# Kernel optimization log

Hardware: AMD Instinct MI355X
Metric: run time of the kernel (lower is better)

## Reference

```python
import jax, jax.numpy as jnp
import numpy as np

DIM = 64      # GCM input_dim
H = DIM // 2  # per-branch width
B = 4         # batch samples
NP = 50000    # points per sample
G = 128       # voxel grid extent
N = B * NP


def _build_coords_and_neighbors():
    rng = np.random.default_rng(0)
    coords = []
    for b in range(B):
        flat = rng.choice(G ** 3, size=NP, replace=False)
        cz = flat % G
        cy = (flat // G) % G
        cx = flat // (G * G)
        coords.append(np.stack([cx, cy, cz], axis=1))
    coords = np.concatenate(coords, axis=0).astype(np.int64)  # [N,3]
    batch_id = np.repeat(np.arange(B), NP).astype(np.int64)
    key = ((batch_id * G + coords[:, 0]) * G + coords[:, 1]) * G + coords[:, 2]
    order = np.argsort(key)
    skey = key[order]
    offs = [(dx, dy, dz) for dx in (-1, 0, 1) for dy in (-1, 0, 1) for dz in (-1, 0, 1)]
    nbr = np.full((27, N), -1, dtype=np.int32)
    for k, (dx, dy, dz) in enumerate(offs):
        nx = coords[:, 0] + dx; ny = coords[:, 1] + dy; nz = coords[:, 2] + dz
        valid = (nx >= 0) & (nx < G) & (ny >= 0) & (ny < G) & (nz >= 0) & (nz < G)
        nkey = ((batch_id * G + nx) * G + ny) * G + nz
        pos = np.searchsorted(skey, nkey)
        pos_c = np.clip(pos, 0, N - 1)
        found = valid & (skey[pos_c] == nkey)
        nbr[k] = np.where(found, order[pos_c], -1).astype(np.int32)
    return nbr, batch_id.astype(np.int32)


def setup_inputs() -> dict:
    nbr, batch_id = _build_coords_and_neighbors()
    key = jax.random.key(0)
    ks = jax.random.split(key, 12)
    sc3 = 1.0 / np.sqrt(27 * H)
    sc1d = 1.0 / np.sqrt(DIM)
    sc1h = 1.0 / np.sqrt(H)
    f32 = jnp.float32
    return {
        "x_feats": jax.random.normal(ks[0], (N, DIM), f32),
        "Wg1": jax.random.normal(ks[1], (DIM, DIM), f32) * sc1d,
        "bg1": jnp.zeros((DIM,), f32),
        "Wg2": jax.random.normal(ks[2], (DIM, DIM), f32) * sc1d,
        "bg2": jnp.zeros((DIM,), f32),
        "Wr1": jax.random.normal(ks[3], (27, H, H), f32) * sc3,
        "br1": jnp.zeros((H,), f32),
        "Wr2": jax.random.normal(ks[4], (27, H, H), f32) * sc3,
        "br2": jnp.zeros((H,), f32),
        "Wq1": jax.random.normal(ks[5], (27, H, H), f32) * sc3,
        "bq1": jnp.zeros((H,), f32),
        "Wq2": jax.random.normal(ks[6], (27, H, H), f32) * sc3,
        "bq2": jnp.zeros((H,), f32),
        "Wq3": jax.random.normal(ks[7], (H, H), f32) * sc1h,
        "bq3": jnp.zeros((H,), f32),
        "nbr_idx": jnp.asarray(nbr),
        "batch_id": jnp.asarray(batch_id),
        "batch_size": B,
    }


def reference(x_feats, Wg1, bg1, Wg2, bg2, Wr1, br1, Wr2, br2,
              Wq1, bq1, Wq2, bq2, Wq3, bq3, nbr_idx, batch_id, batch_size):
    relu = jax.nn.relu

    def sconv(f, W, b):
        # sparse 3x3x3 conv via precomputed kernel maps: out[i] = sum_k f[nbr[k,i]] @ W[k]
        mask = nbr_idx >= 0                                   # [27,N]
        g = jnp.where(mask[:, :, None], f[jnp.clip(nbr_idx, 0)], 0.0)  # [27,N,Cin]
        return jnp.einsum('knc,kco->no', g, W) + b

    # GCM.conv1 (1x1) then channel split
    y = x_feats @ Wg1 + bg1
    conv_x, glo_x = y[:, :H], y[:, H:]

    # resblock (stride=1, no skip conv) + residual in GCM
    r = relu(sconv(conv_x, Wr1, br1))
    r = relu(sconv(r, Wr2, br2))
    conv_x = (r + conv_x) + conv_x

    # glob_feat
    out1 = relu(sconv(glo_x, Wq1, bq1))
    out2 = relu(sconv(glo_x, Wq2, bq2))
    m1 = jnp.mean(out1, axis=1, keepdims=True)                # [N,1]
    sums = jax.ops.segment_sum(out2, batch_id, num_segments=batch_size)  # [B,H]
    cnts = jax.ops.segment_sum(jnp.ones((out2.shape[0], 1), out2.dtype), batch_id,
                               num_segments=batch_size)
    m2 = sums / cnts                                          # per-sample mean over points
    enc = jnp.sqrt(m1 * m2[batch_id] + 1e-12)                 # per-sample outer product
    f = enc + out1 + out2
    f = relu(f @ Wq3 + bq3)
    glo = relu(glo_x - f)

    # GCM.conv2 (1x1) on channel-concat, residual add
    res = jnp.concatenate([conv_x, glo], axis=1) @ Wg2 + bg2
    return x_feats + res
```

## Files before the change

### kernel.cpp

```cpp
#include <hip/hip_runtime.h>
#include <stdint.h>

typedef unsigned int u32;
typedef unsigned short u16;
typedef unsigned long long u64;
typedef __attribute__((ext_vector_type(8))) short bf16x8;
typedef __attribute__((ext_vector_type(4))) float f32x4;

#define HC 32

__device__ __forceinline__ float u2f(u32 u){ union{u32 i;float f;}v; v.i=u; return v.f; }
__device__ __forceinline__ u16 f2bf(float f){ union{float f;u32 i;}v; v.f=f; u32 i=v.i;
    return (u16)((i + 0x7FFFu + ((i>>16)&1u))>>16); }
__device__ __forceinline__ short bfs(float f){ return (short)f2bf(f); }
__device__ __forceinline__ u32 packbf(float a, float b){ return (u32)f2bf(a) | ((u32)f2bf(b)<<16); }

__global__ __launch_bounds__(256) void k0_prep(
    const float* __restrict__ Wq1, const float* __restrict__ Wq2,
    const float* __restrict__ Wr1, const float* __restrict__ Wr2,
    u16* __restrict__ wsB)
{
    int it = blockIdx.x*256 + threadIdx.x;
    if (it >= 216*64) return;
    int l = it & 63, slot = it >> 6;
    int oh = slot & 1, k = (slot >> 1) % 27, mat = slot / 54;
    const float* W = (mat==0)?Wq1:(mat==1)?Wq2:(mat==2)?Wr1:Wr2;
    const float* src = W + k*1024 + oh*16 + (l & 15);
    int crow = (l >> 4) * 8;
    u32 w4[4];
    #pragma unroll
    for (int jj = 0; jj < 4; ++jj)
        w4[jj] = packbf(src[(crow + 2*jj)*32], src[(crow + 2*jj + 1)*32]);
    *(uint4*)&wsB[slot*512 + l*8] = make_uint4(w4[0], w4[1], w4[2], w4[3]);
}

__global__ __launch_bounds__(256) void k1_mfma(
    const float* __restrict__ x, const float* __restrict__ Wg1, const float* __restrict__ bg1,
    float* __restrict__ cv, float* __restrict__ gl, long long N)
{
    const int lane = threadIdx.x & 63;
    const int m = lane & 15, g = lane >> 4;
    bf16x8 bw[4][2];
    #pragma unroll
    for (int no = 0; no < 4; ++no)
      #pragma unroll
      for (int kf = 0; kf < 2; ++kf)
        #pragma unroll
        for (int j = 0; j < 8; ++j)
            bw[no][kf][j] = bfs(Wg1[(kf*32 + g*8 + j)*64 + no*16 + m]);
    float bias4[4];
    #pragma unroll
    for (int no = 0; no < 4; ++no) bias4[no] = bg1[no*16 + m];

    const long long wave = (long long)blockIdx.x*4 + (threadIdx.x>>6);
    long long t0 = wave * 4;
    #pragma unroll 1
    for (long long t = t0; t < t0+4; ++t) {
        long long p0 = t*16;
        if (p0 >= N) break;
        long long pr_a = p0 + m; if (pr_a > N-1) pr_a = N-1;
        const float4* xr = (const float4*)(x + pr_a*64);
        bf16x8 aw[2];
        #pragma unroll
        for (int kf = 0; kf < 2; ++kf) {
            float4 lo = xr[kf*8 + g*2];
            float4 hi = xr[kf*8 + g*2 + 1];
            aw[kf][0]=bfs(lo.x); aw[kf][1]=bfs(lo.y); aw[kf][2]=bfs(lo.z); aw[kf][3]=bfs(lo.w);
            aw[kf][4]=bfs(hi.x); aw[kf][5]=bfs(hi.y); aw[kf][6]=bfs(hi.z); aw[kf][7]=bfs(hi.w);
        }
        #pragma unroll
        for (int no = 0; no < 4; ++no) {
            f32x4 acc = {0.f,0.f,0.f,0.f};
            acc = __builtin_amdgcn_mfma_f32_16x16x32_bf16(aw[0], bw[no][0], acc, 0,0,0);
            acc = __builtin_amdgcn_mfma_f32_16x16x32_bf16(aw[1], bw[no][1], acc, 0,0,0);
            #pragma unroll
            for (int j = 0; j < 4; ++j) {
                long long pr = p0 + g*4 + j;
                if (pr < N) {
                    float v = acc[j] + bias4[no];
                    if (no < 2) cv[pr*32 + no*16 + m] = v;
                    else        gl[pr*32 + (no-2)*16 + m] = v;
                }
            }
        }
    }
}

__device__ __forceinline__ void load_nbr(
    const int* __restrict__ nbr, long long N, long long p0, int lane, int* nbrv)
{
    #pragma unroll
    for (int ch = 0; ch < 7; ++ch) {
        int i = ch*64 + lane;
        int kk = i >> 4, pp = i & 15;
        nbrv[ch] = (i < 432 && p0 + pp < N) ? nbr[(long long)kk*N + p0 + pp] : -1;
    }
}

__device__ __forceinline__ void enum_tile_reg(
    const int* nbrv,
    u16* plist, int* ilist, u16* slist, u16* sstart,
    int lane, u32& np_out, u32& ns_out)
{
    u32 np = 0, ns = 0;
    #pragma unroll
    for (int ch = 0; ch < 7; ++ch) {
        int i = ch*64 + lane;
        int kk = i >> 4, pp = i & 15;
        int ixv = nbrv[ch];
        u64 b = __ballot(ixv >= 0);
        u32 kact = 0;
        #pragma unroll
        for (int q2 = 0; q2 < 4; ++q2)
            kact |= ((((b >> (16*q2)) & 0xffffull) != 0ull) ? 1u : 0u) << q2;
        if (ixv >= 0) {
            u64 ltm = (1ull << lane) - 1ull;
            u32 pos = np + (u32)__popcll(b & ltm);
            int q2 = lane >> 4;
            u32 s = ns + __popc(kact & ((1u << q2) - 1u));
            if (pos < 224) {
                plist[pos] = (u16)((s << 9) | (u32)pp);
                ilist[pos] = ixv;
                u64 subm = 0xffffull << (16*q2);
                if ((b & subm & ltm) == 0ull) { slist[s] = (u16)kk; sstart[s] = (u16)pos; }
            }
        }
        np += (u32)__popcll(b);
        ns += __popc(kact);
    }
    if (np > 224) np = 224;
    np_out = np; ns_out = ns;
}

template<int KAv>
__device__ __forceinline__ void gather_batch(
    const float* __restrict__ src, u16* A,
    const u16* plist, const int* ilist,
    u32 jS, u32 jE, u32 base, int c32, int hf)
{
    constexpr int STR = KAv*32 + 8;
    constexpr int U4R = KAv*4;
    constexpr int NU4 = 16*U4R;
    const int lane = threadIdx.x & 63;
    uint4 z4 = make_uint4(0u,0u,0u,0u);
    #pragma unroll
    for (int w = 0; w < NU4/64; ++w) {
        int q = w*64 + lane;
        int r = q / U4R, c8 = q - r*U4R;
        *(uint4*)&A[r*STR + c8*8] = z4;
    }
    asm volatile("s_waitcnt lgkmcnt(0)" ::: "memory");
    for (u32 j0 = jS; j0 < jE; j0 += 16) {
        float v[8]; u32 mt[8];
        #pragma unroll
        for (int tt = 0; tt < 8; ++tt) {
            u32 pj = j0 + 2*tt + (u32)hf;
            bool val = pj < jE;
            u32 pm = val ? (u32)plist[pj] : 0u;
            int ix = val ? ilist[pj] : 0;
            mt[tt] = val ? (pm | 0x80000000u) : 0u;
            v[tt] = val ? src[(long long)ix*32 + c32] : 0.f;
        }
        #pragma unroll
        for (int tt = 0; tt < 8; ++tt) {
            if (mt[tt] >> 31) {
                u32 sl = ((mt[tt] >> 9) & 31u) - base;
                u32 p = mt[tt] & 15u;
                A[p*STR + sl*32 + c32] = f2bf(v[tt]);
            }
        }
    }
    asm volatile("s_waitcnt lgkmcnt(0)" ::: "memory");
}

template<int KAv>
__device__ __forceinline__ void gather_batch2(
    const float* __restrict__ src0, const float* __restrict__ src1,
    u16* A0, u16* A1,
    const u16* plist, const int* ilist,
    u32 jS, u32 jE, u32 base, int c32, int hf)
{
    constexpr int STR = KAv*32 + 8;
    constexpr int U4R = KAv*4;
    constexpr int NU4 = 16*U4R;
    const int lane = threadIdx.x & 63;
    uint4 z4 = make_uint4(0u,0u,0u,0u);
    #pragma unroll
    for (int w = 0; w < NU4/64; ++w) {
        int q = w*64 + lane;
        int r = q / U4R, c8 = q - r*U4R;
        *(uint4*)&A0[r*STR + c8*8] = z4;
        *(uint4*)&A1[r*STR + c8*8] = z4;
    }
    asm volatile("s_waitcnt lgkmcnt(0)" ::: "memory");
    for (u32 j0 = jS; j0 < jE; j0 += 16) {
        float v0[8], v1[8]; u32 mt[8];
        #pragma unroll
        for (int tt = 0; tt < 8; ++tt) {
            u32 pj = j0 + 2*tt + (u32)hf;
            bool val = pj < jE;
            u32 pm = val ? (u32)plist[pj] : 0u;
            int ix = val ? ilist[pj] : 0;
            mt[tt] = val ? (pm | 0x80000000u) : 0u;
            v0[tt] = val ? src0[(long long)ix*32 + c32] : 0.f;
            v1[tt] = val ? src1[(long long)ix*32 + c32] : 0.f;
        }
        #pragma unroll
        for (int tt = 0; tt < 8; ++tt) {
            if (mt[tt] >> 31) {
                u32 sl = ((mt[tt] >> 9) & 31u) - base;
                u32 p = mt[tt] & 15u;
                A0[p*STR + sl*32 + c32] = f2bf(v0[tt]);
                A1[p*STR + sl*32 + c32] = f2bf(v1[tt]);
            }
        }
    }
    asm volatile("s_waitcnt lgkmcnt(0)" ::: "memory");
}

#define KA2 5
#define STR2 (KA2*32 + 8)
__global__ __launch_bounds__(256, 1) void k2_mfma(
    const float* __restrict__ cv, const float* __restrict__ gl,
    const int* __restrict__ nbr, const int* __restrict__ batch_id,
    const u16* __restrict__ wsB,
    const float* __restrict__ br1, const float* __restrict__ bq1,
    const float* __restrict__ bq2,
    float* __restrict__ r1, float* __restrict__ s12, float* __restrict__ m1,
    float* __restrict__ bsum, long long N)
{
    __shared__ __align__(16) u16 Acv[4][16*STR2];
    __shared__ __align__(16) u16 Agl[4][16*STR2];
    __shared__ u16 plist_s[4][224];
    __shared__ int ilist_s[4][224];
    __shared__ u16 slist_s[4][32];
    __shared__ u16 sstart_s[4][32];
    __shared__ float lbs[128];

    if (threadIdx.x < 128) lbs[threadIdx.x] = 0.f;
    __syncthreads();

    const int wid = threadIdx.x >> 6;
    const int lane = threadIdx.x & 63;
    const int m = lane & 15, g = lane >> 4;
    const int c32 = lane & 31, hf = lane >> 5;
    u16* A0 = Acv[wid];
    u16* A1 = Agl[wid];
    u16* plist = plist_s[wid];
    int* ilist = ilist_s[wid];
    u16* slist = slist_s[wid];
    u16* sstart = sstart_s[wid];

    const float bra = br1[m], brb = br1[16+m];
    const float b1a = bq1[m], b1b = bq1[16+m], b2a = bq2[m], b2b = bq2[16+m];

    const long long ntiles = (N + 15) >> 4;
    const long long tstride = (long long)gridDim.x*4;
    long long t = (long long)blockIdx.x*4 + wid;
    int nbrv[7];
    if (t < ntiles) load_nbr(nbr, N, t*16, lane, nbrv);
    for (; t < ntiles; ) {
        const long long p0 = t*16;
        u32 np, ns;
        enum_tile_reg(nbrv, plist, ilist, slist, sstart, lane, np, ns);
        long long tn = t + tstride;
        if (tn < ntiles) load_nbr(nbr, N, tn*16, lane, nbrv);
        int bb[4];
        #pragma unroll
        for (int j = 0; j < 4; ++j) {
            long long pr = p0 + g*4 + j; if (pr > N-1) pr = N-1;
            bb[j] = batch_id[pr];
        }

        f32x4 accr0 = {0.f,0.f,0.f,0.f}, accr1 = {0.f,0.f,0.f,0.f};
        f32x4 acc10 = {0.f,0.f,0.f,0.f}, acc11 = {0.f,0.f,0.f,0.f};
        f32x4 acc20 = {0.f,0.f,0.f,0.f}, acc21 = {0.f,0.f,0.f,0.f};
        asm volatile("s_waitcnt lgkmcnt(0)" ::: "memory");
        for (u32 base = 0; base < ns; base += KA2) {
            u32 sEnd = base + KA2; if (sEnd > ns) sEnd = ns;
            u32 jS = sstart[base];
            u32 jE = (sEnd < ns) ? (u32)sstart[sEnd] : np;
            gather_batch2<KA2>(cv, gl, A0, A1, plist, ilist, jS, jE, base, c32, hf);
            for (u32 s = base; s < sEnd; ++s) {
                int sl = (int)(s - base);
                int k = slist[s];
                bf16x8 afc = *(const bf16x8*)&A0[m*STR2 + sl*32 + g*8];
                bf16x8 afg = *(const bf16x8*)&A1[m*STR2 + sl*32 + g*8];
                bf16x8 wr0 = *(const bf16x8*)&wsB[(108 + k*2 + 0)*512 + lane*8];
                bf16x8 wr1 = *(const bf16x8*)&wsB[(108 + k*2 + 1)*512 + lane*8];
                bf16x8 w10 = *(const bf16x8*)&wsB[(k*2 + 0)*512 + lane*8];
                bf16x8 w11 = *(const bf16x8*)&wsB[(k*2 + 1)*512 + lane*8];
                bf16x8 w20 = *(const bf16x8*)&wsB[(54 + k*2 + 0)*512 + lane*8];
                bf16x8 w21 = *(const bf16x8*)&wsB[(54 + k*2 + 1)*512 + lane*8];
                accr0 = __builtin_amdgcn_mfma_f32_16x16x32_bf16(afc, wr0, accr0, 0,0,0);
                accr1 = __builtin_amdgcn_mfma_f32_16x16x32_bf16(afc, wr1, accr1, 0,0,0);
                acc10 = __builtin_amdgcn_mfma_f32_16x16x32_bf16(afg, w10, acc10, 0,0,0);
                acc11 = __builtin_amdgcn_mfma_f32_16x16x32_bf16(afg, w11, acc11, 0,0,0);
                acc20 = __builtin_amdgcn_mfma_f32_16x16x32_bf16(afg, w20, acc20, 0,0,0);
                acc21 = __builtin_amdgcn_mfma_f32_16x16x32_bf16(afg, w21, acc21, 0,0,0);
            }
        }
        #pragma unroll
        for (int j = 0; j < 4; ++j) {
            long long pr = p0 + g*4 + j;
            if (pr < N) {
                r1[pr*32 + m]      = fmaxf(accr0[j] + bra, 0.f);
                r1[pr*32 + 16 + m] = fmaxf(accr1[j] + brb, 0.f);
                float o1a = fmaxf(acc10[j] + b1a, 0.f);
                float o1b = fmaxf(acc11[j] + b1b, 0.f);
                float o2a = fmaxf(acc20[j] + b2a, 0.f);
                float o2b = fmaxf(acc21[j] + b2b, 0.f);
                s12[pr*32 + m]      = o1a + o2a;
                s12[pr*32 + 16 + m] = o1b + o2b;
                float rs = o1a + o1b;
                #pragma unroll
                for (int d = 1; d < 16; d <<= 1) rs += __shfl_xor(rs, d, 64);
                if (m == 0) m1[pr] = rs * (1.f/32.f);
                atomicAdd(&lbs[bb[j]*32 + m], o2a);
                atomicAdd(&lbs[bb[j]*32 + 16 + m], o2b);
            }
        }
        t = tn;
    }
    __syncthreads();
    if (threadIdx.x < 128) atomicAdd(&bsum[threadIdx.x], lbs[threadIdx.x]);
}

#define KA3 10
#define STR3 (KA3*32 + 8)
__global__ __launch_bounds__(256, 1) void k3_mfma(
    const float* __restrict__ r1, const float* __restrict__ cv,
    const float* __restrict__ gl, const float* __restrict__ s12,
    const float* __restrict__ m1, const float* __restrict__ bsum,
    const int* __restrict__ nbr, const int* __restrict__ batch_id,
    const u16* __restrict__ wsB, const float* __restrict__ br2,
    const float* __restrict__ Wq3, const float* __restrict__ bq3,
    const float* __restrict__ Wg2, const float* __restrict__ bg2,
    const float* __restrict__ x, float* __restrict__ out,
    long long N, const int* __restrict__ bsz)
{
    __shared__ __align__(16) u16 Acmp[4][16*STR3];
    __shared__ u16 plist_s[4][224];
    __shared__ int ilist_s[4][224];
    __shared__ u16 slist_s[4][32];
    __shared__ u16 sstart_s[4][32];

    const int wid = threadIdx.x >> 6;
    const int lane = threadIdx.x & 63;
    const int m = lane & 15, g = lane >> 4;
    const int c32 = lane & 31, hf = lane >> 5;
    u16* A = Acmp[wid];
    u16* plist = plist_s[wid];
    int* ilist = ilist_s[wid];
    u16* slist = slist_s[wid];
    u16* sstart = sstart_s[wid];
    u16* fin_bf = A;
    u16* a2_bf  = A + 640;

    bf16x8 bq[2];
    #pragma unroll
    for (int no = 0; no < 2; ++no)
      #pragma unroll
      for (int j = 0; j < 8; ++j)
        bq[no][j] = bfs(Wq3[(g*8+j)*32 + no*16 + m]);
    bf16x8 bgw[4][2];
    #pragma unroll
    for (int no = 0; no < 4; ++no)
      #pragma unroll
      for (int kf = 0; kf < 2; ++kf)
        #pragma unroll
        for (int j = 0; j < 8; ++j)
          bgw[no][kf][j] = bfs(Wg2[(kf*32 + g*8 + j)*64 + no*16 + m]);
    const float br2a = br2[m], br2b = br2[16+m];
    const float bq3a = bq3[m], bq3b = bq3[16+m];
    float bgb[4];
    #pragma unroll
    for (int no = 0; no < 4; ++no) bgb[no] = bg2[no*16 + m];
    const float invNP = (float)(*bsz) / (float)N;
    const int p_lin = lane >> 2, c0 = (lane & 3) * 8;

    const long long ntiles = (N + 15) >> 4;
    const long long tstride = (long long)gridDim.x*4;
    long long t = (long long)blockIdx.x*4 + wid;
    int nbrv[7];
    if (t < ntiles) load_nbr(nbr, N, t*16, lane, nbrv);
    for (; t < ntiles; ) {
        const long long p0 = t*16;
        u32 np, ns;
        enum_tile_reg(nbrv, plist, ilist, slist, sstart, lane, np, ns);
        long long tn = t + tstride;
        if (tn < ntiles) load_nbr(nbr, N, tn*16, lane, nbrv);

        float cva[4], cvb[4], gla[4], glb[4], xv[4][4];
        #pragma unroll
        for (int j = 0; j < 4; ++j) {
            int row = g*4 + j;
            long long pr = p0 + row; if (pr > N-1) pr = N-1;
            cva[j] = cv[pr*32 + m];      cvb[j] = cv[pr*32 + 16 + m];
            gla[j] = gl[pr*32 + m];      glb[j] = gl[pr*32 + 16 + m];
            #pragma unroll
            for (int no = 0; no < 4; ++no) xv[no][j] = x[pr*64 + no*16 + m];
        }
        float m1v; float bsv[8], sv[8];
        {
            long long pp = p0 + p_lin; if (pp > N-1) pp = N-1;
            m1v = m1[pp];
            int b = batch_id[pp];
            const float4* bsp = (const float4*)(bsum + b*32 + c0);
            float4 bs0 = bsp[0], bs1 = bsp[1];
            const float4* s12p = (const float4*)(s12 + pp*32 + c0);
            float4 s0 = s12p[0], s1 = s12p[1];
            bsv[0]=bs0.x; bsv[1]=bs0.y; bsv[2]=bs0.z; bsv[3]=bs0.w;
            bsv[4]=bs1.x; bsv[5]=bs1.y; bsv[6]=bs1.z; bsv[7]=bs1.w;
            sv[0]=s0.x; sv[1]=s0.y; sv[2]=s0.z; sv[3]=s0.w;
            sv[4]=s1.x; sv[5]=s1.y; sv[6]=s1.z; sv[7]=s1.w;
        }

        f32x4 acc0 = {0.f,0.f,0.f,0.f}, acc1 = {0.f,0.f,0.f,0.f};
        asm volatile("s_waitcnt lgkmcnt(0)" ::: "memory");
        for (u32 base = 0; base < ns; base += KA3) {
            u32 sEnd = base + KA3; if (sEnd > ns) sEnd = ns;
            u32 jS = sstart[base];
            u32 jE = (sEnd < ns) ? (u32)sstart[sEnd] : np;
            gather_batch<KA3>(r1, A, plist, ilist, jS, jE, base, c32, hf);
            for (u32 s = base; s < sEnd; ++s) {
                int sl = (int)(s - base);
                int k = slist[s];
                bf16x8 af = *(const bf16x8*)&A[m*STR3 + sl*32 + g*8];
                bf16x8 w0 = *(const bf16x8*)&wsB[(162 + k*2 + 0)*512 + lane*8];
                bf16x8 w1 = *(const bf16x8*)&wsB[(162 + k*2 + 1)*512 + lane*8];
                acc0 = __builtin_amdgcn_mfma_f32_16x16x32_bf16(af, w0, acc0, 0,0,0);
                acc1 = __builtin_amdgcn_mfma_f32_16x16x32_bf16(af, w1, acc1, 0,0,0);
            }
        }
        asm volatile("s_waitcnt lgkmcnt(0)" ::: "memory");
        #pragma unroll
        for (int j = 0; j < 4; ++j) {
            int row = g*4 + j;
            a2_bf[row*72 + m]      = f2bf(fmaxf(acc0[j] + br2a, 0.f) + 2.f*cva[j]);
            a2_bf[row*72 + 16 + m] = f2bf(fmaxf(acc1[j] + br2b, 0.f) + 2.f*cvb[j]);
        }
        {
            bf16x8 fbv;
            #pragma unroll
            for (int j = 0; j < 8; ++j) {
                float enc = sqrtf(m1v * bsv[j] * invNP + 1e-12f);
                fbv[j] = bfs(enc + sv[j]);
            }
            *(bf16x8*)&fin_bf[p_lin*40 + c0] = fbv;
        }
        asm volatile("s_waitcnt lgkmcnt(0)" ::: "memory");
        bf16x8 af2 = *(const bf16x8*)&fin_bf[m*40 + g*8];
        f32x4 f0 = {0.f,0.f,0.f,0.f}, f1 = {0.f,0.f,0.f,0.f};
        f0 = __builtin_amdgcn_mfma_f32_16x16x32_bf16(af2, bq[0], f0, 0,0,0);
        f1 = __builtin_amdgcn_mfma_f32_16x16x32_bf16(af2, bq[1], f1, 0,0,0);
        #pragma unroll
        for (int j = 0; j < 4; ++j) {
            int row = g*4 + j;
            float fa = fmaxf(f0[j] + bq3a, 0.f);
            float fb = fmaxf(f1[j] + bq3b, 0.f);
            a2_bf[row*72 + 32 + m] = f2bf(fmaxf(gla[j] - fa, 0.f));
            a2_bf[row*72 + 48 + m] = f2bf(fmaxf(glb[j] - fb, 0.f));
        }
        asm volatile("s_waitcnt lgkmcnt(0)" ::: "memory");
        bf16x8 a20 = *(const bf16x8*)&a2_bf[m*72 + g*8];
        bf16x8 a21 = *(const bf16x8*)&a2_bf[m*72 + 32 + g*8];
        #pragma unroll
        for (int no = 0; no < 4; ++no) {
            f32x4 acc = {0.f,0.f,0.f,0.f};
            acc = __builtin_amdgcn_mfma_f32_16x16x32_bf16(a20, bgw[no][0], acc, 0,0,0);
            acc = __builtin_amdgcn_mfma_f32_16x16x32_bf16(a21, bgw[no][1], acc, 0,0,0);
            #pragma unroll
            for (int j = 0; j < 4; ++j) {
                long long pr = p0 + g*4 + j;
                if (pr < N)
                    out[pr*64 + no*16 + m] = xv[no][j] + acc[j] + bgb[no];
            }
        }
        t = tn;
    }
}

extern "C" void kernel_launch(void* const* d_in, const int* in_sizes, int n_in,
                              void* d_out, int out_size, void* d_ws, size_t ws_size,
                              hipStream_t stream) {
    const float* x   = (const float*)d_in[0];
    const float* Wg1 = (const float*)d_in[1];
    const float* bg1 = (const float*)d_in[2];
    const float* Wg2 = (const float*)d_in[3];
    const float* bg2 = (const float*)d_in[4];
    const float* Wr1 = (const float*)d_in[5];
    const float* br1 = (const float*)d_in[6];
    const float* Wr2 = (const float*)d_in[7];
    const float* br2 = (const float*)d_in[8];
    const float* Wq1 = (const float*)d_in[9];
    const float* bq1 = (const float*)d_in[10];
    const float* Wq2 = (const float*)d_in[11];
    const float* bq2 = (const float*)d_in[12];
    const float* Wq3 = (const float*)d_in[13];
    const float* bq3 = (const float*)d_in[14];
    const int* nbr   = (const int*)d_in[15];
    const int* bid   = (const int*)d_in[16];
    const int* bsz   = (const int*)d_in[17];

    const long long N = (long long)in_sizes[0] / 64;

    float* cv   = (float*)d_ws;
    float* gl   = cv  + N * 32;
    float* r1   = gl  + N * 32;
    float* s12  = r1  + N * 32;
    float* m1   = s12 + N * 32;
    float* bsum = m1  + N;
    u16*   wsB  = (u16*)(bsum + 128);

    float* out = (float*)d_out;

    hipMemsetAsync(bsum, 0, 128 * sizeof(float), stream);

    k0_prep<<<54, 256, 0, stream>>>(Wq1, Wq2, Wr1, Wr2, wsB);

    long long tiles = (N + 15) / 16;
    long long gwaves = (tiles + 3) / 4;
    int gblocks = (int)((gwaves + 3) / 4);
    k1_mfma<<<gblocks, 256, 0, stream>>>(x, Wg1, bg1, cv, gl, N);

    k2_mfma<<<768, 256, 0, stream>>>(cv, gl, nbr, bid, wsB, br1, bq1, bq2,
                                     r1, s12, m1, bsum, N);
    k3_mfma<<<768, 256, 0, stream>>>(r1, cv, gl, s12, m1, bsum, nbr, bid, wsB, br2,
                                     Wq3, bq3, Wg2, bg2, x, out, N, bsz);
}
```

Baseline: 213.3 us.

## Split k2 waves into residual-branch and global-branch specialists per tile

Instead of each wave gathering both cv and gl features for a tile and running all six MFMA chains, waves 0-1 handle only the residual conv (cv, Wr1) and waves 2-3 handle only the glob convs (gl, Wq1/Wq2). Each tile is now processed by two waves, each doing its own neighbor enumeration, with half the LDS A buffer. This lowers per-wave register and LDS pressure and shortens dependency chains, at the cost of duplicating the neighbor load and enumeration work. Load is also uneven, with two MFMA chains on one side and four on the other.

New measurement: 233.5 us. 9.5% more time.

```diff
diff --git a/kernel.cpp b/kernel.cpp
--- a/kernel.cpp
+++ b/kernel.cpp
@@ -173,51 +173,6 @@
     asm volatile("s_waitcnt lgkmcnt(0)" ::: "memory");
 }
 
-template<int KAv>
-__device__ __forceinline__ void gather_batch2(
-    const float* __restrict__ src0, const float* __restrict__ src1,
-    u16* A0, u16* A1,
-    const u16* plist, const int* ilist,
-    u32 jS, u32 jE, u32 base, int c32, int hf)
-{
-    constexpr int STR = KAv*32 + 8;
-    constexpr int U4R = KAv*4;
-    constexpr int NU4 = 16*U4R;
-    const int lane = threadIdx.x & 63;
-    uint4 z4 = make_uint4(0u,0u,0u,0u);
-    #pragma unroll
-    for (int w = 0; w < NU4/64; ++w) {
-        int q = w*64 + lane;
-        int r = q / U4R, c8 = q - r*U4R;
-        *(uint4*)&A0[r*STR + c8*8] = z4;
-        *(uint4*)&A1[r*STR + c8*8] = z4;
-    }
-    asm volatile("s_waitcnt lgkmcnt(0)" ::: "memory");
-    for (u32 j0 = jS; j0 < jE; j0 += 16) {
-        float v0[8], v1[8]; u32 mt[8];
-        #pragma unroll
-        for (int tt = 0; tt < 8; ++tt) {
-            u32 pj = j0 + 2*tt + (u32)hf;
-            bool val = pj < jE;
-            u32 pm = val ? (u32)plist[pj] : 0u;
-            int ix = val ? ilist[pj] : 0;
-            mt[tt] = val ? (pm | 0x80000000u) : 0u;
-            v0[tt] = val ? src0[(long long)ix*32 + c32] : 0.f;
-            v1[tt] = val ? src1[(long long)ix*32 + c32] : 0.f;
-        }
-        #pragma unroll
-        for (int tt = 0; tt < 8; ++tt) {
-            if (mt[tt] >> 31) {
-                u32 sl = ((mt[tt] >> 9) & 31u) - base;
-                u32 p = mt[tt] & 15u;
-                A0[p*STR + sl*32 + c32] = f2bf(v0[tt]);
-                A1[p*STR + sl*32 + c32] = f2bf(v1[tt]);
-            }
-        }
-    }
-    asm volatile("s_waitcnt lgkmcnt(0)" ::: "memory");
-}
-
 #define KA2 5
 #define STR2 (KA2*32 + 8)
 __global__ __launch_bounds__(256, 1) void k2_mfma(
@@ -229,8 +184,7 @@
     float* __restrict__ r1, float* __restrict__ s12, float* __restrict__ m1,
     float* __restrict__ bsum, long long N)
 {
-    __shared__ __align__(16) u16 Acv[4][16*STR2];
-    __shared__ __align__(16) u16 Agl[4][16*STR2];
+    __shared__ __align__(16) u16 Abuf[4][16*STR2];
     __shared__ u16 plist_s[4][224];
     __shared__ int ilist_s[4][224];
     __shared__ u16 slist_s[4][32];
@@ -244,83 +198,114 @@
     const int lane = threadIdx.x & 63;
     const int m = lane & 15, g = lane >> 4;
     const int c32 = lane & 31, hf = lane >> 5;
-    u16* A0 = Acv[wid];
-    u16* A1 = Agl[wid];
+    u16* A = Abuf[wid];
     u16* plist = plist_s[wid];
     int* ilist = ilist_s[wid];
     u16* slist = slist_s[wid];
     u16* sstart = sstart_s[wid];
 
-    const float bra = br1[m], brb = br1[16+m];
-    const float b1a = bq1[m], b1b = bq1[16+m], b2a = bq2[m], b2b = bq2[16+m];
-
     const long long ntiles = (N + 15) >> 4;
-    const long long tstride = (long long)gridDim.x*4;
-    long long t = (long long)blockIdx.x*4 + wid;
-    int nbrv[7];
-    if (t < ntiles) load_nbr(nbr, N, t*16, lane, nbrv);
-    for (; t < ntiles; ) {
-        const long long p0 = t*16;
-        u32 np, ns;
-        enum_tile_reg(nbrv, plist, ilist, slist, sstart, lane, np, ns);
-        long long tn = t + tstride;
-        if (tn < ntiles) load_nbr(nbr, N, tn*16, lane, nbrv);
-        int bb[4];
-        #pragma unroll
-        for (int j = 0; j < 4; ++j) {
-            long long pr = p0 + g*4 + j; if (pr > N-1) pr = N-1;
-            bb[j] = batch_id[pr];
-        }
-
-        f32x4 accr0 = {0.f,0.f,0.f,0.f}, accr1 = {0.f,0.f,0.f,0.f};
-        f32x4 acc10 = {0.f,0.f,0.f,0.f}, acc11 = {0.f,0.f,0.f,0.f};
-        f32x4 acc20 = {0.f,0.f,0.f,0.f}, acc21 = {0.f,0.f,0.f,0.f};
-        asm volatile("s_waitcnt lgkmcnt(0)" ::: "memory");
-        for (u32 base = 0; base < ns; base += KA2) {
-            u32 sEnd = base + KA2; if (sEnd > ns) sEnd = ns;
-            u32 jS = sstart[base];
-            u32 jE = (sEnd < ns) ? (u32)sstart[sEnd] : np;
-            gather_batch2<KA2>(cv, gl, A0, A1, plist, ilist, jS, jE, base, c32, hf);
-            for (u32 s = base; s < sEnd; ++s) {
-                int sl = (int)(s - base);
-                int k = slist[s];
-                bf16x8 afc = *(const bf16x8*)&A0[m*STR2 + sl*32 + g*8];
-                bf16x8 afg = *(const bf16x8*)&A1[m*STR2 + sl*32 + g*8];
-                bf16x8 wr0 = *(const bf16x8*)&wsB[(108 + k*2 + 0)*512 + lane*8];
-                bf16x8 wr1 = *(const bf16x8*)&wsB[(108 + k*2 + 1)*512 + lane*8];
-                bf16x8 w10 = *(const bf16x8*)&wsB[(k*2 + 0)*512 + lane*8];
-                bf16x8 w11 = *(const bf16x8*)&wsB[(k*2 + 1)*512 + lane*8];
-                bf16x8 w20 = *(const bf16x8*)&wsB[(54 + k*2 + 0)*512 + lane*8];
-                bf16x8 w21 = *(const bf16x8*)&wsB[(54 + k*2 + 1)*512 + lane*8];
-                accr0 = __builtin_amdgcn_mfma_f32_16x16x32_bf16(afc, wr0, accr0, 0,0,0);
-                accr1 = __builtin_amdgcn_mfma_f32_16x16x32_bf16(afc, wr1, accr1, 0,0,0);
-                acc10 = __builtin_amdgcn_mfma_f32_16x16x32_bf16(afg, w10, acc10, 0,0,0);
-                acc11 = __builtin_amdgcn_mfma_f32_16x16x32_bf16(afg, w11, acc11, 0,0,0);
-                acc20 = __builtin_amdgcn_mfma_f32_16x16x32_bf16(afg, w20, acc20, 0,0,0);
-                acc21 = __builtin_amdgcn_mfma_f32_16x16x32_bf16(afg, w21, acc21, 0,0,0);
-            }
-        }
-        #pragma unroll
-        for (int j = 0; j < 4; ++j) {
-            long long pr = p0 + g*4 + j;
-            if (pr < N) {
-                r1[pr*32 + m]      = fmaxf(accr0[j] + bra, 0.f);
-                r1[pr*32 + 16 + m] = fmaxf(accr1[j] + brb, 0.f);
-                float o1a = fmaxf(acc10[j] + b1a, 0.f);
-                float o1b = fmaxf(acc11[j] + b1b, 0.f);
-                float o2a = fmaxf(acc20[j] + b2a, 0.f);
-                float o2b = fmaxf(acc21[j] + b2b, 0.f);
-                s12[pr*32 + m]      = o1a + o2a;
-                s12[pr*32 + 16 + m] = o1b + o2b;
-                float rs = o1a + o1b;
-                #pragma unroll
-                for (int d = 1; d < 16; d <<= 1) rs += __shfl_xor(rs, d, 64);
-                if (m == 0) m1[pr] = rs * (1.f/32.f);
-                atomicAdd(&lbs[bb[j]*32 + m], o2a);
-                atomicAdd(&lbs[bb[j]*32 + 16 + m], o2b);
-            }
-        }
-        t = tn;
+    const long long tstride = (long long)gridDim.x*2;
+
+    if (wid < 2) {
+        const float bra = br1[m], brb = br1[16+m];
+        long long t = (long long)blockIdx.x*2 + wid;
+        int nbrv[7];
+        if (t < ntiles) load_nbr(nbr, N, t*16, lane, nbrv);
+        for (; t < ntiles; ) {
+            const long long p0 = t*16;
+            u32 np, ns;
+            enum_tile_reg(nbrv, plist, ilist, slist, sstart, lane, np, ns);
+            long long tn = t + tstride;
+            if (tn < ntiles) load_nbr(nbr, N, tn*16, lane, nbrv);
+
+            f32x4 accr0 = {0.f,0.f,0.f,0.f}, accr1 = {0.f,0.f,0.f,0.f};
+            asm volatile("s_waitcnt lgkmcnt(0)" ::: "memory");
+            for (u32 base = 0; base < ns; base += KA2) {
+                u32 sEnd = base + KA2; if (sEnd > ns) sEnd = ns;
+                u32 jS = sstart[base];
+                u32 jE = (sEnd < ns) ? (u32)sstart[sEnd] : np;
+                gather_batch<KA2>(cv, A, plist, ilist, jS, jE, base, c32, hf);
+                for (u32 s = base; s < sEnd; ++s) {
+                    int sl = (int)(s - base);
+                    int k = slist[s];
+                    bf16x8 af  = *(const bf16x8*)&A[m*STR2 + sl*32 + g*8];
+                    bf16x8 wr0 = *(const bf16x8*)&wsB[(108 + k*2 + 0)*512 + lane*8];
+                    bf16x8 wr1v = *(const bf16x8*)&wsB[(108 + k*2 + 1)*512 + lane*8];
+                    accr0 = __builtin_amdgcn_mfma_f32_16x16x32_bf16(af, wr0, accr0, 0,0,0);
+                    accr1 = __builtin_amdgcn_mfma_f32_16x16x32_bf16(af, wr1v, accr1, 0,0,0);
+                }
+            }
+            #pragma unroll
+            for (int j = 0; j < 4; ++j) {
+                long long pr = p0 + g*4 + j;
+                if (pr < N) {
+                    r1[pr*32 + m]      = fmaxf(accr0[j] + bra, 0.f);
+                    r1[pr*32 + 16 + m] = fmaxf(accr1[j] + brb, 0.f);
+                }
+            }
+            t = tn;
+        }
+    } else {
+        const float b1a = bq1[m], b1b = bq1[16+m], b2a = bq2[m], b2b = bq2[16+m];
+        long long t = (long long)blockIdx.x*2 + (wid - 2);
+        int nbrv[7];
+        if (t < ntiles) load_nbr(nbr, N, t*16, lane, nbrv);
+        for (; t < ntiles; ) {
+            const long long p0 = t*16;
+            u32 np, ns;
+            enum_tile_reg(nbrv, plist, ilist, slist, sstart, lane, np, ns);
+            long long tn = t + tstride;
+            if (tn < ntiles) load_nbr(nbr, N, tn*16, lane, nbrv);
+            int bb[4];
+            #pragma unroll
+            for (int j = 0; j < 4; ++j) {
+                long long pr = p0 + g*4 + j; if (pr > N-1) pr = N-1;
+                bb[j] = batch_id[pr];
+            }
+
+            f32x4 acc10 = {0.f,0.f,0.f,0.f}, acc11 = {0.f,0.f,0.f,0.f};
+            f32x4 acc20 = {0.f,0.f,0.f,0.f}, acc21 = {0.f,0.f,0.f,0.f};
+            asm volatile("s_waitcnt lgkmcnt(0)" ::: "memory");
+            for (u32 base = 0; base < ns; base += KA2) {
+                u32 sEnd = base + KA2; if (sEnd > ns) sEnd = ns;
+                u32 jS = sstart[base];
+                u32 jE = (sEnd < ns) ? (u32)sstart[sEnd] : np;
+                gather_batch<KA2>(gl, A, plist, ilist, jS, jE, base, c32, hf);
+                for (u32 s = base; s < sEnd; ++s) {
+                    int sl = (int)(s - base);
+                    int k = slist[s];
+                    bf16x8 af  = *(const bf16x8*)&A[m*STR2 + sl*32 + g*8];
+                    bf16x8 w10 = *(const bf16x8*)&wsB[(k*2 + 0)*512 + lane*8];
+                    bf16x8 w11 = *(const bf16x8*)&wsB[(k*2 + 1)*512 + lane*8];
+                    bf16x8 w20 = *(const bf16x8*)&wsB[(54 + k*2 + 0)*512 + lane*8];
+                    bf16x8 w21 = *(const bf16x8*)&wsB[(54 + k*2 + 1)*512 + lane*8];
+                    acc10 = __builtin_amdgcn_mfma_f32_16x16x32_bf16(af, w10, acc10, 0,0,0);
+                    acc11 = __builtin_amdgcn_mfma_f32_16x16x32_bf16(af, w11, acc11, 0,0,0);
+                    acc20 = __builtin_amdgcn_mfma_f32_16x16x32_bf16(af, w20, acc20, 0,0,0);
+                    acc21 = __builtin_amdgcn_mfma_f32_16x16x32_bf16(af, w21, acc21, 0,0,0);
+                }
+            }
+            #pragma unroll
+            for (int j = 0; j < 4; ++j) {
+                long long pr = p0 + g*4 + j;
+                if (pr < N) {
+                    float o1a = fmaxf(acc10[j] + b1a, 0.f);
+                    float o1b = fmaxf(acc11[j] + b1b, 0.f);
+                    float o2a = fmaxf(acc20[j] + b2a, 0.f);
+                    float o2b = fmaxf(acc21[j] + b2b, 0.f);
+                    s12[pr*32 + m]      = o1a + o2a;
+                    s12[pr*32 + 16 + m] = o1b + o2b;
+                    float rs = o1a + o1b;
+                    #pragma unroll
+                    for (int d = 1; d < 16; d <<= 1) rs += __shfl_xor(rs, d, 64);
+                    if (m == 0) m1[pr] = rs * (1.f/32.f);
+                    atomicAdd(&lbs[bb[j]*32 + m], o2a);
+                    atomicAdd(&lbs[bb[j]*32 + 16 + m], o2b);
+                }
+            }
+            t = tn;
+        }
     }
     __syncthreads();
     if (threadIdx.x < 128) atomicAdd(&bsum[threadIdx.x], lbs[threadIdx.x]);
```
